# Kernel optimization log

Hardware: AMD Instinct MI355X
Metric: run time of the kernel (lower is better)

## Reference

```python
import jax, jax.numpy as jnp
import numpy as np

BT, H, V = 4096, 2048, 32000
BETA = 0.5
TEMPERATURE = 1.0
W_SCALE = 0.02  # keep logits in a sane range so softmax is not saturated


def setup_inputs() -> dict:
    key = jax.random.key(0)
    k1, k2, k3, k4 = jax.random.split(key, 4)
    return {
        "student_input": jax.random.normal(k1, (BT, H), dtype=jnp.float32),
        "teacher_input": jax.random.normal(k2, (BT, H), dtype=jnp.float32),
        "w_student": jax.random.normal(k3, (V, H), dtype=jnp.float32) * W_SCALE,
        "w_teacher": jax.random.normal(k4, (V, H), dtype=jnp.float32) * W_SCALE,
    }


def reference(student_input, teacher_input, w_student, w_teacher):
    # Fused linear + generalized Jensen-Shannon divergence (Liger semantics).
    # logits = x @ W.T, temperature-scaled before softmax.
    s_logits = jnp.einsum("nh,vh->nv", student_input, w_student) / TEMPERATURE
    t_logits = jnp.einsum("nh,vh->nv", teacher_input, w_teacher) / TEMPERATURE
    log_q = jax.nn.log_softmax(s_logits, axis=-1)  # student
    log_p = jax.nn.log_softmax(t_logits, axis=-1)  # teacher
    p = jnp.exp(log_p)
    q = jnp.exp(log_q)
    m = BETA * p + (1.0 - BETA) * q
    log_m = jnp.log(m)
    # JSD_beta(P || Q) = beta*KL(P||M) + (1-beta)*KL(Q||M), mean over tokens
    loss = BETA * jnp.sum(p * (log_p - log_m)) + (1.0 - BETA) * jnp.sum(q * (log_q - log_m))
    return loss / BT
```

## Files before the change

kernel.cpp:

```cpp
#include <hip/hip_runtime.h>
#include <cstdint>

#define BT 4096
#define HD 2048
#define VD 32000

typedef __attribute__((ext_vector_type(4))) float float4_t;
typedef __attribute__((ext_vector_type(4))) short short4_t;
typedef __attribute__((ext_vector_type(8))) short short8_t;
typedef __attribute__((ext_vector_type(8))) unsigned short ushort8_t;
typedef __attribute__((ext_vector_type(2))) long long2_t;
typedef __attribute__((ext_vector_type(4))) unsigned int uint4_t;

constexpr int BM = 128, BN = 128, BK = 32;

__device__ __forceinline__ unsigned short f2bf(float f) {
  unsigned u = __float_as_uint(f);
  u += 0x7FFFu + ((u >> 16) & 1u);
  return (unsigned short)(u >> 16);
}

__device__ __forceinline__ float bf2f(unsigned short h) {
  return __uint_as_float((unsigned)h << 16);
}

__device__ __forceinline__ short8_t pack8(float4_t a, float4_t b) {
  short8_t h;
  h[0] = (short)f2bf(a.x); h[1] = (short)f2bf(a.y);
  h[2] = (short)f2bf(a.z); h[3] = (short)f2bf(a.w);
  h[4] = (short)f2bf(b.x); h[5] = (short)f2bf(b.y);
  h[6] = (short)f2bf(b.z); h[7] = (short)f2bf(b.w);
  return h;
}

__device__ __forceinline__ void async_copy16(const void* g, void* l) {
  __builtin_amdgcn_global_load_lds(
      (__attribute__((address_space(1))) void*)(uintptr_t)(g),
      (__attribute__((address_space(3))) void*)(uint32_t)(uintptr_t)(l),
      16, 0, 0);
}

__global__ __launch_bounds__(256) void cast_f32_to_bf16(
    const float4_t* __restrict__ in, short4_t* __restrict__ out, int n4) {
  for (int i = blockIdx.x * 256 + threadIdx.x; i < n4; i += gridDim.x * 256) {
    float4_t v = in[i];
    short4_t o;
    o.x = (short)f2bf(v.x); o.y = (short)f2bf(v.y);
    o.z = (short)f2bf(v.z); o.w = (short)f2bf(v.w);
    out[i] = o;
  }
}

__device__ __forceinline__ unsigned int pk_fp8x4(float a, float b, float c, float d) {
  int p = __builtin_amdgcn_cvt_pk_fp8_f32(a, b, 0, false);
  p = __builtin_amdgcn_cvt_pk_fp8_f32(c, d, p, true);
  return (unsigned int)p;
}

__global__ __launch_bounds__(256) void cast_all_fp8i(
    const float* __restrict__ xs, const float* __restrict__ xt,
    const float* __restrict__ ws, const float* __restrict__ wt,
    uint4_t* __restrict__ oxs, uint4_t* __restrict__ oxt,
    uint4_t* __restrict__ ows, uint4_t* __restrict__ owt,
    float* __restrict__ out) {
  const long XP = (long)BT * HD / 16;
  const long WP = (long)VD * HD / 16;
  const long total = 2 * (XP + WP);
  const long i0 = blockIdx.x * 256L + threadIdx.x;
  if (i0 == 0) out[0] = 0.6931471805599453f;
  for (long i = i0; i < total; i += gridDim.x * 256L) {
    const float* s; uint4_t* d; float scl; long j = i;
    if (j < XP) { s = xs; d = oxs; scl = 1.f; }
    else if ((j -= XP) < XP) { s = xt; d = oxt; scl = 1.f; }
    else if ((j -= XP) < WP) { s = ws; d = ows; scl = 64.f; }
    else { j -= WP; s = wt; d = owt; scl = 64.f; }
    const float* sp = s + ((j >> 2) * 64 + (j & 3) * 8);
    float4_t v0 = *(const float4_t*)(sp);
    float4_t v1 = *(const float4_t*)(sp + 4);
    float4_t v2 = *(const float4_t*)(sp + 32);
    float4_t v3 = *(const float4_t*)(sp + 36);
    uint4_t o;
    o.x = pk_fp8x4(v0.x * scl, v0.y * scl, v0.z * scl, v0.w * scl);
    o.y = pk_fp8x4(v1.x * scl, v1.y * scl, v1.z * scl, v1.w * scl);
    o.z = pk_fp8x4(v2.x * scl, v2.y * scl, v2.z * scl, v2.w * scl);
    o.w = pk_fp8x4(v3.x * scl, v3.y * scl, v3.z * scl, v3.w * scl);
    d[j] = o;
  }
}

__device__ __forceinline__ int swz(int row) { return (row ^ (row >> 2)) & 3; }

template <bool F32SRC>
__device__ __forceinline__ void ktile(const void* A, const void* B,
                                      float4_t (&acc)[4][4],
                                      unsigned short* As, unsigned short* Bs,
                                      int m0, int n0) {
  const int tid = threadIdx.x;
  const int lane = tid & 63;
  const int wave = tid >> 6;
  const int wm = wave >> 1, wn = wave & 1;
  const int r0 = tid >> 2, c0 = tid & 3;
  const int cg = c0 ^ swz(r0);
  const int row16 = lane & 15, kq = lane >> 4;
  const int kqs = kq ^ swz(row16);
  const int aoff = (wm * 64 + row16) * BK + kqs * 8;
  const int boff = (wn * 64 + row16) * BK + kqs * 8;
  const int lds0 = __builtin_amdgcn_readfirstlane(wave * 1024);
  const int lds1 = __builtin_amdgcn_readfirstlane(4096 + wave * 1024);

  const unsigned short* Ab = nullptr; const unsigned short* Bb = nullptr;
  const float* Af = nullptr; const float* Bf = nullptr;
  if constexpr (!F32SRC) {
    Ab = (const unsigned short*)A + (size_t)(m0 + r0) * HD + cg * 8;
    Bb = (const unsigned short*)B + (size_t)(n0 + r0) * HD + cg * 8;
  } else {
    Af = (const float*)A + (size_t)(m0 + r0) * HD + cg * 8;
    Bf = (const float*)B + (size_t)(n0 + r0) * HD + cg * 8;
  }

  for (int kb = 0; kb < HD / BK; ++kb) {
    const int ke = kb * BK;
    if constexpr (!F32SRC) {
      async_copy16(Ab + ke, (char*)As + lds0);
      async_copy16(Ab + (size_t)64 * HD + ke, (char*)As + lds1);
      async_copy16(Bb + ke, (char*)Bs + lds0);
      async_copy16(Bb + (size_t)64 * HD + ke, (char*)Bs + lds1);
    } else {
      short8_t hA0 = pack8(*(const float4_t*)(Af + ke), *(const float4_t*)(Af + ke + 4));
      short8_t hA1 = pack8(*(const float4_t*)(Af + (size_t)64 * HD + ke),
                           *(const float4_t*)(Af + (size_t)64 * HD + ke + 4));
      short8_t hB0 = pack8(*(const float4_t*)(Bf + ke), *(const float4_t*)(Bf + ke + 4));
      short8_t hB1 = pack8(*(const float4_t*)(Bf + (size_t)64 * HD + ke),
                           *(const float4_t*)(Bf + (size_t)64 * HD + ke + 4));
      *(short8_t*)((char*)As + tid * 16) = hA0;
      *(short8_t*)((char*)As + 4096 + tid * 16) = hA1;
      *(short8_t*)((char*)Bs + tid * 16) = hB0;
      *(short8_t*)((char*)Bs + 4096 + tid * 16) = hB1;
    }
    __syncthreads();
    short8_t af[4], bfv[4];
#pragma unroll
    for (int mi = 0; mi < 4; ++mi) af[mi] = *(const short8_t*)(As + aoff + mi * 16 * BK);
#pragma unroll
    for (int ni = 0; ni < 4; ++ni) bfv[ni] = *(const short8_t*)(Bs + boff + ni * 16 * BK);
#pragma unroll
    for (int mi = 0; mi < 4; ++mi)
#pragma unroll
      for (int ni = 0; ni < 4; ++ni)
        acc[mi][ni] = __builtin_amdgcn_mfma_f32_16x16x32_bf16(af[mi], bfv[ni], acc[mi][ni], 0, 0, 0);
    __syncthreads();
  }
}

template <bool F32SRC, bool STORE>
__global__ __launch_bounds__(256, 2) void gemm_pass1(
    const void* A0, const void* A1, const void* B0, const void* B1,
    float* __restrict__ rowsum, unsigned short* __restrict__ store) {
  __shared__ __align__(16) unsigned short As[BM * BK];
  __shared__ __align__(16) unsigned short Bs[BN * BK];
  const int m0 = blockIdx.x * BM;
  const int n0 = blockIdx.y * BN;
  const int z = blockIdx.z;
  const void* A = z ? A1 : A0;
  const void* B = z ? B1 : B0;
  float4_t acc[4][4] = {};
  ktile<F32SRC>(A, B, acc, As, Bs, m0, n0);

  const int tid = threadIdx.x;
  const int lane = tid & 63;
  const int wave = tid >> 6;
  const int wm = wave >> 1, wn = wave & 1;
  const int row16 = lane & 15, kq = lane >> 4;

  if constexpr (STORE) {
    unsigned short* st = store + (size_t)z * BT * VD;
#pragma unroll
    for (int mi = 0; mi < 4; ++mi)
#pragma unroll
      for (int r = 0; r < 4; ++r) {
        const size_t grow = (size_t)(m0 + wm * 64 + mi * 16 + kq * 4 + r);
        const size_t gc0 = (size_t)(n0 + wn * 64 + row16);
#pragma unroll
        for (int ni = 0; ni < 4; ++ni)
          st[grow * VD + gc0 + ni * 16] = f2bf(acc[mi][ni][r]);
      }
  }

  float* rs = rowsum + z * BT;
#pragma unroll
  for (int mi = 0; mi < 4; ++mi)
#pragma unroll
    for (int r = 0; r < 4; ++r) {
      float s = __expf(acc[mi][0][r]) + __expf(acc[mi][1][r]) +
                __expf(acc[mi][2][r]) + __expf(acc[mi][3][r]);
      s += __shfl_xor(s, 1);
      s += __shfl_xor(s, 2);
      s += __shfl_xor(s, 4);
      s += __shfl_xor(s, 8);
      if (row16 == 0) atomicAdd(&rs[m0 + wm * 64 + mi * 16 + kq * 4 + r], s);
    }
}

constexpr int NKT8 = HD / 64;

__global__ __launch_bounds__(256, 3) void gemm128_fp8_pass1(
    const unsigned char* __restrict__ fXs, const unsigned char* __restrict__ fXt,
    const unsigned char* __restrict__ fWs, const unsigned char* __restrict__ fWt,
    float* __restrict__ rowsum, unsigned short* __restrict__ store) {
  __shared__ __align__(16) unsigned char lds8[2 * 16384];

  const int z = blockIdx.y;
  const unsigned char* A = z ? fXt : fXs;
  const unsigned char* B = z ? fWt : fWs;

  const int o = blockIdx.x;
  const int s = (o & 7) * 1000 + (o >> 3);
  const int m0 = (s & 31) * 128;
  const int n0 = (s >> 5) * 128;

  const int tid = threadIdx.x;
  const int lane = tid & 63;
  const int wave = tid >> 6;
  const int wm = wave >> 1;
  const int wn = wave & 1;
  const int row16 = lane & 15, kq = lane >> 4;
  const int rh = row16 >> 1;
  const int cA = (((row16 & 1) << 2) | kq) ^ rh;

  const int lr = lane >> 3, lc = lane & 7;
  const int cl = lc ^ lr;
  const int k16 = (cl & 3) * 16;
  const int mloc0 = (wave * 2 + 0) * 16 + 2 * lr + (cl >> 2);
  const int mloc1 = (wave * 2 + 1) * 16 + 2 * lr + (cl >> 2);
  const unsigned char* srcA0 = A + (size_t)(m0 + mloc0) * HD + k16;
  const unsigned char* srcA1 = A + (size_t)(m0 + mloc1) * HD + k16;
  const unsigned char* srcB0 = B + (size_t)(n0 + mloc0) * HD + k16;
  const unsigned char* srcB1 = B + (size_t)(n0 + mloc1) * HD + k16;
  const int stA0 = __builtin_amdgcn_readfirstlane((wave * 2 + 0) * 1024);
  const int stA1 = __builtin_amdgcn_readfirstlane((wave * 2 + 1) * 1024);

#define STAGE(ktv, sl)                                                   \
  do {                                                                   \
    char* _sb = (char*)lds8 + (sl) * 16384;                              \
    async_copy16(srcA0 + (size_t)(ktv) * 64, _sb + stA0);                \
    async_copy16(srcA1 + (size_t)(ktv) * 64, _sb + stA1);                \
    async_copy16(srcB0 + (size_t)(ktv) * 64, _sb + 8192 + stA0);         \
    async_copy16(srcB1 + (size_t)(ktv) * 64, _sb + 8192 + stA1);         \
  } while (0)

  STAGE(0, 0);
  asm volatile("s_waitcnt vmcnt(0)" ::: "memory");
  __builtin_amdgcn_s_barrier();

  float4_t acc[4][4] = {};
  const int aoff = (wm * 32 + rh) * 128 + cA * 16;
  const int boff = (wn * 32 + rh) * 128 + cA * 16;

#pragma unroll 1
  for (int kt = 0; kt < NKT8; ++kt) {
    __builtin_amdgcn_sched_barrier(0);
    const int ktS = (kt + 1 > NKT8 - 1) ? NKT8 - 1 : kt + 1;
    STAGE(ktS, (kt + 1) & 1);

    const unsigned char* Asl = lds8 + (kt & 1) * 16384;
    const unsigned char* Bsl = Asl + 8192;
    long2_t a[4], b[4];
#pragma unroll
    for (int mi = 0; mi < 4; ++mi) a[mi] = *(const long2_t*)(Asl + aoff + mi * 1024);
#pragma unroll
    for (int ni = 0; ni < 4; ++ni) b[ni] = *(const long2_t*)(Bsl + boff + ni * 1024);

    __builtin_amdgcn_s_setprio(1);
#pragma unroll
    for (int mi = 0; mi < 4; ++mi)
#pragma unroll
      for (int ni = 0; ni < 4; ++ni)
        acc[mi][ni] = __builtin_amdgcn_mfma_f32_16x16x32_fp8_fp8(a[mi].x, b[ni].x, acc[mi][ni], 0, 0, 0);
#pragma unroll
    for (int mi = 0; mi < 4; ++mi)
#pragma unroll
      for (int ni = 0; ni < 4; ++ni)
        acc[mi][ni] = __builtin_amdgcn_mfma_f32_16x16x32_fp8_fp8(a[mi].y, b[ni].y, acc[mi][ni], 0, 0, 0);
    __builtin_amdgcn_s_setprio(0);

    asm volatile("s_waitcnt vmcnt(0)" ::: "memory");
    __builtin_amdgcn_s_barrier();
  }
#undef STAGE

  const float SCL = 0.015625f;
  unsigned short* st = store + (size_t)z * BT * VD;
  float* rs = rowsum + z * BT;
#pragma unroll
  for (int mi = 0; mi < 4; ++mi)
#pragma unroll
    for (int r = 0; r < 4; ++r) {
      const size_t grow = (size_t)(m0 + wm * 64 + mi * 16 + kq * 4 + r);
      const size_t gc0 = (size_t)(n0 + wn * 64 + row16);
      float zv[4];
#pragma unroll
      for (int ni = 0; ni < 4; ++ni) {
        zv[ni] = acc[mi][ni][r] * SCL;
        st[grow * VD + gc0 + ni * 16] = f2bf(zv[ni]);
      }
      float ssum = __expf(zv[0]) + __expf(zv[1]) + __expf(zv[2]) + __expf(zv[3]);
      ssum += __shfl_xor(ssum, 1);
      ssum += __shfl_xor(ssum, 2);
      ssum += __shfl_xor(ssum, 4);
      ssum += __shfl_xor(ssum, 8);
      if (row16 == 0) atomicAdd(&rs[grow], ssum);
    }
}

__global__ __launch_bounds__(256) void lse_fix(float* __restrict__ stats,
                                               float* __restrict__ out) {
  const int i = blockIdx.x * 256 + threadIdx.x;
  if (i < 2 * BT) stats[i] = __logf(stats[i]);
  if (i == 0) out[0] = 0.6931471805599453f;
}

__global__ void seed_out(float* __restrict__ out) {
  out[0] = 0.6931471805599453f;
}

__global__ __launch_bounds__(256) void loss_from_blogits(
    const ushort8_t* __restrict__ zs, const ushort8_t* __restrict__ zt,
    const float* __restrict__ rs, float* __restrict__ out) {
  const int row = blockIdx.x;
  const float es = __logf(rs[row]), et = __logf(rs[BT + row]);
  const ushort8_t* ps = zs + (size_t)row * (VD / 8);
  const ushort8_t* pt = zt + (size_t)row * (VD / 8);
  float local = 0.f;
  for (int i = threadIdx.x; i < VD / 8; i += 256) {
    const ushort8_t a = ps[i], b = pt[i];
#pragma unroll
    for (int c = 0; c < 8; ++c) {
      const float ls = bf2f(a[c]) - es, lt = bf2f(b[c]) - et;
      const float p = __expf(ls), q = __expf(lt);
      local += p * ls + q * lt - (p + q) * __logf(p + q);
    }
  }
  local += __shfl_xor(local, 1);
  local += __shfl_xor(local, 2);
  local += __shfl_xor(local, 4);
  local += __shfl_xor(local, 8);
  local += __shfl_xor(local, 16);
  local += __shfl_xor(local, 32);
  __shared__ float red[4];
  const int lane = threadIdx.x & 63, wave = threadIdx.x >> 6;
  if (lane == 0) red[wave] = local;
  __syncthreads();
  if (threadIdx.x == 0)
    atomicAdd(out, (red[0] + red[1] + red[2] + red[3]) * (0.5f / BT));
}

template <bool F32SRC>
__global__ __launch_bounds__(256, 2) void gemm_loss(
    const void* Asg, const void* Bsg, const void* Atg, const void* Btg,
    const float* __restrict__ lse, float* __restrict__ out) {
  __shared__ __align__(16) unsigned short As[BM * BK];
  __shared__ __align__(16) unsigned short Bs[BN * BK];
  __shared__ float red[4];
  const int m0 = blockIdx.x * BM;
  const int n0 = blockIdx.y * BN;
  float4_t acc_s[4][4] = {};
  ktile<F32SRC>(Asg, Bsg, acc_s, As, Bs, m0, n0);
  float4_t acc_t[4][4] = {};
  ktile<F32SRC>(Atg, Btg, acc_t, As, Bs, m0, n0);

  const int tid = threadIdx.x;
  const int lane = tid & 63;
  const int wave = tid >> 6;
  const int wm = wave >> 1;
  const int kq = lane >> 4;

  float local = 0.f;
#pragma unroll
  for (int mi = 0; mi < 4; ++mi)
#pragma unroll
    for (int r = 0; r < 4; ++r) {
      const int grow = m0 + wm * 64 + mi * 16 + kq * 4 + r;
      const float es = lse[grow], et = lse[BT + grow];
#pragma unroll
      for (int ni = 0; ni < 4; ++ni) {
        const float ls = acc_s[mi][ni][r] - es;
        const float lt = acc_t[mi][ni][r] - et;
        const float p = __expf(ls), q = __expf(lt);
        local += p * ls + q * lt - (p + q) * __logf(p + q);
      }
    }
  local += __shfl_xor(local, 1);
  local += __shfl_xor(local, 2);
  local += __shfl_xor(local, 4);
  local += __shfl_xor(local, 8);
  local += __shfl_xor(local, 16);
  local += __shfl_xor(local, 32);
  if (lane == 0) red[wave] = local;
  __syncthreads();
  if (tid == 0) atomicAdd(out, (red[0] + red[1] + red[2] + red[3]) * (0.5f / BT));
}

extern "C" void kernel_launch(void* const* d_in, const int* in_sizes, int n_in,
                              void* d_out, int out_size, void* d_ws, size_t ws_size,
                              hipStream_t stream) {
  const float* Xs = (const float*)d_in[0];
  const float* Xt = (const float*)d_in[1];
  const float* Ws = (const float*)d_in[2];
  const float* Wt = (const float*)d_in[3];
  float* out = (float*)d_out;
  char* ws = (char*)d_ws;

  const size_t STATS_B = (size_t)2 * BT * sizeof(float);
  const size_t XB8 = (size_t)BT * HD;
  const size_t WB8 = (size_t)VD * HD;
  const size_t XB = (size_t)BT * HD * 2;
  const size_t WB = (size_t)VD * HD * 2;
  const size_t LOGIT_B = (size_t)2 * BT * VD * 2;
  const size_t FP8_NEED = STATS_B + 2 * XB8 + 2 * WB8 + LOGIT_B;
  const size_t PRECAST_NEED = STATS_B + 2 * XB + 2 * WB;
  const size_t MID_NEED = STATS_B + LOGIT_B;

  float* stats = (float*)ws;
  hipMemsetAsync(stats, 0, STATS_B, stream);

  const dim3 blk(256);
  const dim3 g1(BT / BM, VD / BN, 2);
  const dim3 g2(BT / BM, VD / BN, 1);
  const int XN4 = BT * HD / 4;
  const int WN4 = VD * HD / 4;

  if (ws_size >= FP8_NEED) {
    unsigned char* fXs = (unsigned char*)(ws + STATS_B);
    unsigned char* fXt = fXs + XB8;
    unsigned char* fWs = fXt + XB8;
    unsigned char* fWt = fWs + WB8;
    unsigned short* logits = (unsigned short*)(ws + STATS_B + 2 * XB8 + 2 * WB8);
    cast_all_fp8i<<<dim3(2048), blk, 0, stream>>>(
        Xs, Xt, Ws, Wt,
        (uint4_t*)fXs, (uint4_t*)fXt, (uint4_t*)fWs, (uint4_t*)fWt, out);
    gemm128_fp8_pass1<<<dim3((BT / 128) * (VD / 128), 2), dim3(256), 0, stream>>>(
        fXs, fXt, fWs, fWt, stats, logits);
    loss_from_blogits<<<dim3(BT), blk, 0, stream>>>(
        (const ushort8_t*)logits,
        (const ushort8_t*)(logits + (size_t)BT * VD), stats, out);
  } else if (ws_size >= MID_NEED) {
    unsigned short* logits = (unsigned short*)(ws + STATS_B);
    gemm_pass1<true, true><<<g1, blk, 0, stream>>>(Xs, Xt, Ws, Wt, stats, logits);
    seed_out<<<dim3(1), dim3(1), 0, stream>>>(out);
    loss_from_blogits<<<dim3(BT), blk, 0, stream>>>(
        (const ushort8_t*)logits,
        (const ushort8_t*)(logits + (size_t)BT * VD), stats, out);
  } else if (ws_size >= PRECAST_NEED) {
    unsigned short* bXs = (unsigned short*)(ws + STATS_B);
    unsigned short* bXt = bXs + (size_t)BT * HD;
    unsigned short* bWs = bXt + (size_t)BT * HD;
    unsigned short* bWt = bWs + (size_t)VD * HD;
    cast_f32_to_bf16<<<dim3(512), blk, 0, stream>>>((const float4_t*)Xs, (short4_t*)bXs, XN4);
    cast_f32_to_bf16<<<dim3(512), blk, 0, stream>>>((const float4_t*)Xt, (short4_t*)bXt, XN4);
    cast_f32_to_bf16<<<dim3(2048), blk, 0, stream>>>((const float4_t*)Ws, (short4_t*)bWs, WN4);
    cast_f32_to_bf16<<<dim3(2048), blk, 0, stream>>>((const float4_t*)Wt, (short4_t*)bWt, WN4);
    gemm_pass1<false, false><<<g1, blk, 0, stream>>>(bXs, bXt, bWs, bWt, stats, nullptr);
    lse_fix<<<dim3(32), blk, 0, stream>>>(stats, out);
    gemm_loss<false><<<g2, blk, 0, stream>>>(bXs, bWs, bXt, bWt, stats, out);
  } else {
    gemm_pass1<true, false><<<g1, blk, 0, stream>>>(Xs, Xt, Ws, Wt, stats, nullptr);
    lse_fix<<<dim3(32), blk, 0, stream>>>(stats, out);
    gemm_loss<true><<<g2, blk, 0, stream>>>(Xs, Ws, Xt, Wt, stats, out);
  }
  (void)in_sizes; (void)n_in; (void)out_size;
}
```

Before: 1.442 ms.

## Use MX-scaled 16x16x128 FP8 MFMA with doubled K tile in pass1 GEMM

Replaces the pair of 16x16x32 FP8 MFMAs per k-step with the gfx950 scaled 16x16x128 f8f6f4 MFMA, using unit scales (0x7F). The K tile per iteration doubles to 128, LDS staging doubles to 64KB, and occupancy drops from 3 to 2 blocks per CU. The aim is higher matrix-core throughput per instruction and half as many loop iterations and barriers. The cost is more LDS pressure and lower occupancy. The fragment assembly from two 64-byte LDS halves must also match the K ordering the instruction expects.

```diff
diff --git a/kernel.cpp b/kernel.cpp
--- a/kernel.cpp
+++ b/kernel.cpp
@@ -9,8 +9,9 @@
 typedef __attribute__((ext_vector_type(4))) short short4_t;
 typedef __attribute__((ext_vector_type(8))) short short8_t;
 typedef __attribute__((ext_vector_type(8))) unsigned short ushort8_t;
-typedef __attribute__((ext_vector_type(2))) long long2_t;
 typedef __attribute__((ext_vector_type(4))) unsigned int uint4_t;
+typedef __attribute__((ext_vector_type(4))) int int4v;
+typedef __attribute__((ext_vector_type(8))) int int8v;
 
 constexpr int BM = 128, BN = 128, BK = 32;
 
@@ -201,13 +202,13 @@
     }
 }
 
-constexpr int NKT8 = HD / 64;
-
-__global__ __launch_bounds__(256, 3) void gemm128_fp8_pass1(
+constexpr int NKT16 = HD / 128;
+
+__global__ __launch_bounds__(256, 2) void gemm128_mx_pass1(
     const unsigned char* __restrict__ fXs, const unsigned char* __restrict__ fXt,
     const unsigned char* __restrict__ fWs, const unsigned char* __restrict__ fWt,
     float* __restrict__ rowsum, unsigned short* __restrict__ store) {
-  __shared__ __align__(16) unsigned char lds8[2 * 16384];
+  __shared__ __align__(16) unsigned char lds8[2 * 32768];
 
   const int z = blockIdx.y;
   const unsigned char* A = z ? fXt : fXs;
@@ -239,13 +240,18 @@
   const int stA0 = __builtin_amdgcn_readfirstlane((wave * 2 + 0) * 1024);
   const int stA1 = __builtin_amdgcn_readfirstlane((wave * 2 + 1) * 1024);
 
-#define STAGE(ktv, sl)                                                   \
-  do {                                                                   \
-    char* _sb = (char*)lds8 + (sl) * 16384;                              \
-    async_copy16(srcA0 + (size_t)(ktv) * 64, _sb + stA0);                \
-    async_copy16(srcA1 + (size_t)(ktv) * 64, _sb + stA1);                \
-    async_copy16(srcB0 + (size_t)(ktv) * 64, _sb + 8192 + stA0);         \
-    async_copy16(srcB1 + (size_t)(ktv) * 64, _sb + 8192 + stA1);         \
+#define STAGE(ktv, sl)                                                    \
+  do {                                                                    \
+    char* _sb = (char*)lds8 + (sl) * 32768;                               \
+    const size_t _k0 = (size_t)(ktv) * 128;                               \
+    async_copy16(srcA0 + _k0, _sb + stA0);                                \
+    async_copy16(srcA1 + _k0, _sb + stA1);                                \
+    async_copy16(srcA0 + _k0 + 64, _sb + 8192 + stA0);                    \
+    async_copy16(srcA1 + _k0 + 64, _sb + 8192 + stA1);                    \
+    async_copy16(srcB0 + _k0, _sb + 16384 + stA0);                        \
+    async_copy16(srcB1 + _k0, _sb + 16384 + stA1);                        \
+    async_copy16(srcB0 + _k0 + 64, _sb + 24576 + stA0);                   \
+    async_copy16(srcB1 + _k0 + 64, _sb + 24576 + stA1);                   \
   } while (0)
 
   STAGE(0, 0);
@@ -257,30 +263,34 @@
   const int boff = (wn * 32 + rh) * 128 + cA * 16;
 
 #pragma unroll 1
-  for (int kt = 0; kt < NKT8; ++kt) {
+  for (int kt = 0; kt < NKT16; ++kt) {
     __builtin_amdgcn_sched_barrier(0);
-    const int ktS = (kt + 1 > NKT8 - 1) ? NKT8 - 1 : kt + 1;
+    const int ktS = (kt + 1 > NKT16 - 1) ? NKT16 - 1 : kt + 1;
     STAGE(ktS, (kt + 1) & 1);
 
-    const unsigned char* Asl = lds8 + (kt & 1) * 16384;
-    const unsigned char* Bsl = Asl + 8192;
-    long2_t a[4], b[4];
-#pragma unroll
-    for (int mi = 0; mi < 4; ++mi) a[mi] = *(const long2_t*)(Asl + aoff + mi * 1024);
-#pragma unroll
-    for (int ni = 0; ni < 4; ++ni) b[ni] = *(const long2_t*)(Bsl + boff + ni * 1024);
+    const unsigned char* Asl = lds8 + (kt & 1) * 32768;
+    const unsigned char* Bsl = Asl + 16384;
+    int8v a[4], b[4];
+#pragma unroll
+    for (int mi = 0; mi < 4; ++mi) {
+      int4v lo = *(const int4v*)(Asl + aoff + mi * 1024);
+      int4v hi = *(const int4v*)(Asl + 8192 + aoff + mi * 1024);
+      a[mi] = (int8v){lo.x, lo.y, lo.z, lo.w, hi.x, hi.y, hi.z, hi.w};
+    }
+#pragma unroll
+    for (int ni = 0; ni < 4; ++ni) {
+      int4v lo = *(const int4v*)(Bsl + boff + ni * 1024);
+      int4v hi = *(const int4v*)(Bsl + 8192 + boff + ni * 1024);
+      b[ni] = (int8v){lo.x, lo.y, lo.z, lo.w, hi.x, hi.y, hi.z, hi.w};
+    }
 
     __builtin_amdgcn_s_setprio(1);
 #pragma unroll
     for (int mi = 0; mi < 4; ++mi)
 #pragma unroll
       for (int ni = 0; ni < 4; ++ni)
-        acc[mi][ni] = __builtin_amdgcn_mfma_f32_16x16x32_fp8_fp8(a[mi].x, b[ni].x, acc[mi][ni], 0, 0, 0);
-#pragma unroll
-    for (int mi = 0; mi < 4; ++mi)
-#pragma unroll
-      for (int ni = 0; ni < 4; ++ni)
-        acc[mi][ni] = __builtin_amdgcn_mfma_f32_16x16x32_fp8_fp8(a[mi].y, b[ni].y, acc[mi][ni], 0, 0, 0);
+        acc[mi][ni] = __builtin_amdgcn_mfma_scale_f32_16x16x128_f8f6f4(
+            a[mi], b[ni], acc[mi][ni], 0, 0, 0, 0x7F, 0, 0x7F);
     __builtin_amdgcn_s_setprio(0);
 
     asm volatile("s_waitcnt vmcnt(0)" ::: "memory");
@@ -438,7 +448,7 @@
     cast_all_fp8i<<<dim3(2048), blk, 0, stream>>>(
         Xs, Xt, Ws, Wt,
         (uint4_t*)fXs, (uint4_t*)fXt, (uint4_t*)fWs, (uint4_t*)fWt, out);
-    gemm128_fp8_pass1<<<dim3((BT / 128) * (VD / 128), 2), dim3(256), 0, stream>>>(
+    gemm128_mx_pass1<<<dim3((BT / 128) * (VD / 128), 2), dim3(256), 0, stream>>>(
         fXs, fXt, fWs, fWt, stats, logits);
     loss_from_blogits<<<dim3(BT), blk, 0, stream>>>(
         (const ushort8_t*)logits,
```

After: 1.503 ms. 1.04x slower.
